# Kernel optimization log

Measured on AMD Instinct MI355X. Metric: run time of the kernel, lower is better.

## Reference

```python
import jax, jax.numpy as jnp
import numpy as np


def setup_inputs() -> dict:
    key = jax.random.key(0)
    k1, k2 = jax.random.split(key)
    x = jax.random.normal(k1, (8, 8192, 512), dtype=jnp.float32)
    codebook = jax.random.normal(k2, (1024, 512), dtype=jnp.float32)
    return {"x": x, "codebook": codebook}


def reference(x, codebook):
    # torch.cdist -> Euclidean distance; argmin is invariant under sqrt, so
    x2 = jnp.sum(x * x, axis=-1, keepdims=True)          # [B, N, 1]
    c2 = jnp.sum(codebook * codebook, axis=-1)           # [K]
    xc = jnp.einsum('bnd,kd->bnk', x, codebook)          # [B, N, K]
    d2 = x2 - 2.0 * xc + c2                              # [B, N, K]
    idx = jnp.argmin(d2, axis=-1)                        # [B, N]
    return codebook[idx]                                 # [B, N, dim]
```

## Files before the change

### kernel.cpp

```cpp
#include <hip/hip_runtime.h>
#include <cstdio>


typedef float f32x4 __attribute__((ext_vector_type(4)));
typedef _Float16 half8 __attribute__((ext_vector_type(8)));

#define KDIM 512
#define NCODES 1024
#define NQ 65536
#define TAU_S 0.05f

#define WS_CBH   0ull
#define WS_C2H   1048576ull
#define WS_C2D   1052672ull
#define WS_CBT   1060864ull
#define WS_IDX   3158016ull
#define WS_LIST  3420160ull
#define WS_CTR   3682304ull
#define WS_NEED  (WS_CTR + 4ull)

__device__ __forceinline__ unsigned short f2h(float f) {
  _Float16 h = (_Float16)f;
  return __builtin_bit_cast(unsigned short, h);
}

__device__ __forceinline__ void async16(const void* g, void* l) {
  __builtin_amdgcn_global_load_lds(
      (const __attribute__((address_space(1))) void*)g,
      (__attribute__((address_space(3))) void*)l, 16, 0, 0);
}

__global__ __launch_bounds__(256) void vq_prep(const float* __restrict__ cb,
                                               unsigned short* __restrict__ cbh,
                                               float* __restrict__ c2h,
                                               double* __restrict__ c2d) {
  int lane = threadIdx.x & 63;
  int row = blockIdx.x * 4 + (threadIdx.x >> 6);
  const float4* src = (const float4*)(cb + (size_t)row * KDIM);
  float4 u = src[lane * 2], v = src[lane * 2 + 1];
  double p = (double)u.x * u.x + (double)u.y * u.y + (double)u.z * u.z + (double)u.w * u.w +
             (double)v.x * v.x + (double)v.y * v.y + (double)v.z * v.z + (double)v.w * v.w;
#pragma unroll
  for (int m = 1; m < 64; m <<= 1) p += __shfl_xor(p, m);
  if (lane == 0) { c2h[row] = (float)(0.5 * p); c2d[row] = 0.5 * p; }
  unsigned r0 = f2h(u.x) | ((unsigned)f2h(u.y) << 16);
  unsigned r1 = f2h(u.z) | ((unsigned)f2h(u.w) << 16);
  unsigned r2 = f2h(v.x) | ((unsigned)f2h(v.y) << 16);
  unsigned r3 = f2h(v.z) | ((unsigned)f2h(v.w) << 16);
  *(int4*)(cbh + (size_t)row * KDIM + lane * 8) = make_int4((int)r0, (int)r1, (int)r2, (int)r3);
}

__global__ __launch_bounds__(512, 2) void vq_main(const float* __restrict__ x,
                                                  const unsigned short* __restrict__ cbh,
                                                  const float* __restrict__ c2h,
                                                  int* __restrict__ idx,
                                                  int* __restrict__ list,
                                                  int* __restrict__ counter) {
  __shared__ __align__(16) char pool[135168];
  float* c2s = (float*)(pool + 131072);

  const int tid = threadIdx.x;
  const int lane = tid & 63, wv = tid >> 6;
  const int c = lane & 15, q = lane >> 4;
  const int qbase = blockIdx.x * 256 + wv * 32;

#define STAGE(cc) do {                                                        \
    const unsigned short* _s = cbh + (size_t)(cc) * 32768 + wv * 4096;        \
    char* _d = pool + (((cc) & 1) * 65536) + wv * 8192 + lane * 16;           \
    _Pragma("unroll")                                                         \
    for (int s = 0; s < 8; ++s)                                               \
      async16(_s + s * 512 + ((lane ^ s) * 8), _d + s * 1024); } while (0)

  if (wv < 4) async16(c2h + (wv * 64 + lane) * 4, pool + 131072 + wv * 1024 + lane * 16);
  STAGE(0);

  half8 a[2][16];
  {
    const float* xr0 = x + (size_t)(qbase + c) * KDIM + q * 8;
    const float* xr1 = xr0 + (size_t)16 * KDIM;
    float4 t0[8], t1[8];
#pragma unroll
    for (int gj = 0; gj < 4; ++gj) {
      const float* p = xr0 + gj * 32;
      t0[gj * 2] = *(const float4*)p;
      t0[gj * 2 + 1] = *(const float4*)(p + 4);
    }
#pragma unroll
    for (int g = 0; g < 8; ++g) {
      if (g + 1 < 8) {
#pragma unroll
        for (int gj = 0; gj < 4; ++gj) {
          const int fi = (g + 1) * 4 + gj;
          const int rf = fi >> 4, kf = fi & 15;
          const float* p = (rf ? xr1 : xr0) + kf * 32;
          if ((g + 1) & 1) {
            t1[gj * 2] = *(const float4*)p; t1[gj * 2 + 1] = *(const float4*)(p + 4);
          } else {
            t0[gj * 2] = *(const float4*)p; t0[gj * 2 + 1] = *(const float4*)(p + 4);
          }
        }
      }
#pragma unroll
      for (int gj = 0; gj < 4; ++gj) {
        const int fi = g * 4 + gj;
        const int rf = fi >> 4, kf = fi & 15;
        float4 lo, hi;
        if (g & 1) { lo = t1[gj * 2]; hi = t1[gj * 2 + 1]; }
        else       { lo = t0[gj * 2]; hi = t0[gj * 2 + 1]; }
        half8 h;
        h[0] = (_Float16)lo.x; h[1] = (_Float16)lo.y;
        h[2] = (_Float16)lo.z; h[3] = (_Float16)lo.w;
        h[4] = (_Float16)hi.x; h[5] = (_Float16)hi.y;
        h[6] = (_Float16)hi.z; h[7] = (_Float16)hi.w;
        a[rf][kf] = h;
      }
      __builtin_amdgcn_sched_barrier(0);
    }
  }

  float m1[2][4], m2[2][4];
  int mcx[2][4];
#pragma unroll
  for (int i = 0; i < 2; ++i)
#pragma unroll
    for (int r = 0; r < 4; ++r) { m1[i][r] = 1e30f; m2[i][r] = 1e30f; mcx[i][r] = 0; }

  const int crow = c * 512;
  const int m3 = c & 7;

#pragma unroll 1
  for (int ch = 0; ch < 16; ++ch) {
    __syncthreads();
    if (ch + 1 < 16) STAGE(ch + 1);

    const unsigned short* B = (const unsigned short*)(pool + ((ch & 1) * 65536));
    f32x4 acc[2][4];
#pragma unroll
    for (int i = 0; i < 2; ++i)
#pragma unroll
      for (int j = 0; j < 4; ++j) acc[i][j] = (f32x4){0.f, 0.f, 0.f, 0.f};

#pragma unroll
    for (int kf = 0; kf < 16; ++kf) {
      half8 b[4];
      const int gg = (kf * 4 + q) ^ m3;
#pragma unroll
      for (int cf = 0; cf < 4; ++cf)
        b[cf] = *(const half8*)&B[cf * 8192 + crow + gg * 8];
#pragma unroll
      for (int i = 0; i < 2; ++i)
#pragma unroll
        for (int cf = 0; cf < 4; ++cf)
          acc[i][cf] = __builtin_amdgcn_mfma_f32_16x16x32_f16(a[i][kf], b[cf], acc[i][cf], 0, 0, 0);
    }
#pragma unroll
    for (int cf = 0; cf < 4; ++cf) {
      const int col = ch * 64 + cf * 16 + c;
      const float c2v = c2s[col];
#pragma unroll
      for (int i = 0; i < 2; ++i)
#pragma unroll
        for (int r = 0; r < 4; ++r) {
          float sv = c2v - acc[i][cf][r];
          float hi = fmaxf(sv, m1[i][r]);
          m2[i][r] = fminf(m2[i][r], hi);
          bool lt = sv < m1[i][r];
          m1[i][r] = lt ? sv : m1[i][r];
          mcx[i][r] = lt ? col : mcx[i][r];
        }
    }
  }
#undef STAGE

#pragma unroll
  for (int m = 1; m < 16; m <<= 1) {
#pragma unroll
    for (int i = 0; i < 2; ++i)
#pragma unroll
      for (int r = 0; r < 4; ++r) {
        float o1 = __shfl_xor(m1[i][r], m);
        float o2 = __shfl_xor(m2[i][r], m);
        int   oc = __shfl_xor(mcx[i][r], m);
        float hi = fmaxf(o1, m1[i][r]);
        m2[i][r] = fminf(fminf(m2[i][r], o2), hi);
        bool lt = o1 < m1[i][r];
        m1[i][r] = lt ? o1 : m1[i][r];
        mcx[i][r] = lt ? oc : mcx[i][r];
      }
  }
  if (c == 0) {
#pragma unroll
    for (int i = 0; i < 2; ++i)
#pragma unroll
      for (int r = 0; r < 4; ++r) {
        int query = qbase + i * 16 + q * 4 + r;
        idx[query] = mcx[i][r];
        if (m2[i][r] - m1[i][r] < TAU_S) { int p = atomicAdd(counter, 1); list[p] = query; }
      }
  }
}

__global__ __launch_bounds__(256) void vq_trans(const float4* __restrict__ cb4,
                                                float4* __restrict__ cbT4) {
  __shared__ float t[64][65];
  const int bc = blockIdx.x >> 3, bk = blockIdx.x & 7;
  const int c0 = bc * 64, k0 = bk * 64;
  const int r = threadIdx.x >> 4, q4 = threadIdx.x & 15;
#pragma unroll
  for (int p = 0; p < 4; ++p) {
    int row = p * 16 + r;
    float4 v = cb4[(size_t)(c0 + row) * 128 + (k0 >> 2) + q4];
    t[row][q4 * 4 + 0] = v.x; t[row][q4 * 4 + 1] = v.y;
    t[row][q4 * 4 + 2] = v.z; t[row][q4 * 4 + 3] = v.w;
  }
  __syncthreads();
#pragma unroll
  for (int p = 0; p < 4; ++p) {
    int kk = p * 16 + r;
    float4 v = make_float4(t[q4 * 4 + 0][kk], t[q4 * 4 + 1][kk],
                           t[q4 * 4 + 2][kk], t[q4 * 4 + 3][kk]);
    cbT4[(size_t)(k0 + kk) * 256 + (c0 >> 2) + q4] = v;
  }
}

__global__ __launch_bounds__(256) void vq_refine(const float* __restrict__ x,
                                                 const float4* __restrict__ cbT4,
                                                 const double* __restrict__ c2d,
                                                 const int* __restrict__ list,
                                                 const int* __restrict__ counter,
                                                 int* __restrict__ idx) {
  __shared__ __align__(16) float xs[8][512];
  __shared__ int qlist[8];
  __shared__ double rv[8][4];
  __shared__ int rc[8][4];
  const int cnt = counter[0];
  const int tid = threadIdx.x, lane = tid & 63, wv = tid >> 6;
  for (int base = blockIdx.x * 8; base < cnt; base += gridDim.x * 8) {
    const int nq = min(8, cnt - base);
    __syncthreads();
    if (tid < 8) qlist[tid] = list[base + ((tid < nq) ? tid : 0)];
    __syncthreads();
#pragma unroll
    for (int k = 0; k < 4; ++k) {
      int e = tid + 256 * k;
      int qi = e >> 7, d4 = e & 127;
      ((float4*)xs)[e] = ((const float4*)(x + (size_t)qlist[qi] * KDIM))[d4];
    }
    __syncthreads();
    double a0[8], a1[8], a2[8], a3[8];
#pragma unroll
    for (int qi = 0; qi < 8; ++qi) { a0[qi] = 0; a1[qi] = 0; a2[qi] = 0; a3[qi] = 0; }
#pragma unroll 2
    for (int k4 = 0; k4 < 128; ++k4) {
      float4 c0 = cbT4[(k4 * 4 + 0) * 256 + tid];
      float4 c1 = cbT4[(k4 * 4 + 1) * 256 + tid];
      float4 c2v = cbT4[(k4 * 4 + 2) * 256 + tid];
      float4 c3 = cbT4[(k4 * 4 + 3) * 256 + tid];
#pragma unroll
      for (int qi = 0; qi < 8; ++qi) {
        float4 xv = *(const float4*)&xs[qi][k4 * 4];
        a0[qi] = fma((double)xv.x, (double)c0.x, a0[qi]);
        a1[qi] = fma((double)xv.x, (double)c0.y, a1[qi]);
        a2[qi] = fma((double)xv.x, (double)c0.z, a2[qi]);
        a3[qi] = fma((double)xv.x, (double)c0.w, a3[qi]);
        a0[qi] = fma((double)xv.y, (double)c1.x, a0[qi]);
        a1[qi] = fma((double)xv.y, (double)c1.y, a1[qi]);
        a2[qi] = fma((double)xv.y, (double)c1.z, a2[qi]);
        a3[qi] = fma((double)xv.y, (double)c1.w, a3[qi]);
        a0[qi] = fma((double)xv.z, (double)c2v.x, a0[qi]);
        a1[qi] = fma((double)xv.z, (double)c2v.y, a1[qi]);
        a2[qi] = fma((double)xv.z, (double)c2v.z, a2[qi]);
        a3[qi] = fma((double)xv.z, (double)c2v.w, a3[qi]);
        a0[qi] = fma((double)xv.w, (double)c3.x, a0[qi]);
        a1[qi] = fma((double)xv.w, (double)c3.y, a1[qi]);
        a2[qi] = fma((double)xv.w, (double)c3.z, a2[qi]);
        a3[qi] = fma((double)xv.w, (double)c3.w, a3[qi]);
      }
    }
    const double c2l0 = c2d[tid * 4], c2l1 = c2d[tid * 4 + 1];
    const double c2l2 = c2d[tid * 4 + 2], c2l3 = c2d[tid * 4 + 3];
#pragma unroll
    for (int qi = 0; qi < 8; ++qi) {
      double best = c2l0 - a0[qi];
      int bc = tid * 4;
      double s1 = c2l1 - a1[qi];
      if (s1 < best) { best = s1; bc = tid * 4 + 1; }
      double s2 = c2l2 - a2[qi];
      if (s2 < best) { best = s2; bc = tid * 4 + 2; }
      double s3 = c2l3 - a3[qi];
      if (s3 < best) { best = s3; bc = tid * 4 + 3; }
#pragma unroll
      for (int m = 1; m < 64; m <<= 1) {
        double o = __shfl_xor(best, m);
        int oc = __shfl_xor(bc, m);
        if (o < best) { best = o; bc = oc; }
      }
      if (lane == 0) { rv[qi][wv] = best; rc[qi][wv] = bc; }
    }
    __syncthreads();
    if (tid < nq) {
      double b = rv[tid][0];
      int bci = rc[tid][0];
#pragma unroll
      for (int w = 1; w < 4; ++w)
        if (rv[tid][w] < b) { b = rv[tid][w]; bci = rc[tid][w]; }
      idx[qlist[tid]] = bci;
    }
  }
}

__global__ __launch_bounds__(256) void vq_gather(const float* __restrict__ cb,
                                                 const int* __restrict__ idx,
                                                 float* __restrict__ out) {
  size_t i = (size_t)blockIdx.x * 256 + threadIdx.x;
  int qg = (int)(i >> 7), d = (int)(i & 127);
  ((float4*)out)[i] = ((const float4*)cb)[(size_t)idx[qg] * 128 + d];
}

extern "C" void kernel_launch(void* const* d_in, const int* in_sizes, int n_in,
                              void* d_out, int out_size, void* d_ws, size_t ws_size,
                              hipStream_t stream) {
  const float* x = (const float*)d_in[0];
  const float* cb = (const float*)d_in[1];
  float* out = (float*)d_out;
  char* ws = (char*)d_ws;
  if (ws_size < WS_NEED) {
    fprintf(stderr, "vq: ws_size %zu too small (need %llu)\n", ws_size,
            (unsigned long long)WS_NEED);
    return;
  }
  unsigned short* cbh = (unsigned short*)(ws + WS_CBH);
  float* c2h = (float*)(ws + WS_C2H);
  double* c2d = (double*)(ws + WS_C2D);
  float* cbT = (float*)(ws + WS_CBT);
  int* idx = (int*)(ws + WS_IDX);
  int* list = (int*)(ws + WS_LIST);
  int* counter = (int*)(ws + WS_CTR);

  hipMemsetAsync(counter, 0, 4, stream);
  vq_prep<<<256, 256, 0, stream>>>(cb, cbh, c2h, c2d);
  vq_trans<<<128, 256, 0, stream>>>((const float4*)cb, (float4*)cbT);
  vq_main<<<256, 512, 0, stream>>>(x, cbh, c2h, idx, list, counter);
  vq_refine<<<2048, 256, 0, stream>>>(x, (const float4*)cbT, c2d, list, counter, idx);
  vq_gather<<<32768, 256, 0, stream>>>(cb, idx, out);
}
```

Before: 418.6 us.

## Give each wave 64 queries in main kernel and simplify refine to one query per block

The main kernel drops to 4 waves per block, and each wave now computes 64 queries instead of 32. This doubles the reuse of every codebook fragment read from LDS but raises register pressure (a[4][16] and acc[4][4]). The x preload loses its software-pipelined double buffering, and staging is rewritten so each wave copies 16 rows. The refine kernel now handles one query per block instead of batching 8, which drops cross-query reuse of the transposed codebook loads.

```diff
diff --git a/kernel.cpp b/kernel.cpp
--- a/kernel.cpp
+++ b/kernel.cpp
@@ -50,7 +50,7 @@
   *(int4*)(cbh + (size_t)row * KDIM + lane * 8) = make_int4((int)r0, (int)r1, (int)r2, (int)r3);
 }
 
-__global__ __launch_bounds__(512, 2) void vq_main(const float* __restrict__ x,
+__global__ __launch_bounds__(256, 1) void vq_main(const float* __restrict__ x,
                                                   const unsigned short* __restrict__ cbh,
                                                   const float* __restrict__ c2h,
                                                   int* __restrict__ idx,
@@ -62,70 +62,51 @@
   const int tid = threadIdx.x;
   const int lane = tid & 63, wv = tid >> 6;
   const int c = lane & 15, q = lane >> 4;
-  const int qbase = blockIdx.x * 256 + wv * 32;
+  const int qbase = blockIdx.x * 256 + wv * 64;
 
 #define STAGE(cc) do {                                                        \
-    const unsigned short* _s = cbh + (size_t)(cc) * 32768 + wv * 4096;        \
-    char* _d = pool + (((cc) & 1) * 65536) + wv * 8192 + lane * 16;           \
+    const unsigned short* _s = cbh + (size_t)(cc) * 32768;                    \
+    char* _d = pool + (((cc) & 1) * 65536);                                   \
     _Pragma("unroll")                                                         \
-    for (int s = 0; s < 8; ++s)                                               \
-      async16(_s + s * 512 + ((lane ^ s) * 8), _d + s * 1024); } while (0)
-
-  if (wv < 4) async16(c2h + (wv * 64 + lane) * 4, pool + 131072 + wv * 1024 + lane * 16);
+    for (int s = 0; s < 16; ++s) {                                            \
+      int r = wv * 16 + s;                                                    \
+      async16(_s + (size_t)r * 512 + ((lane ^ (r & 7)) * 8),                  \
+              _d + r * 1024 + lane * 16);                                     \
+    } } while (0)
+
+  async16(c2h + wv * 256 + lane * 4, pool + 131072 + wv * 1024 + lane * 16);
   STAGE(0);
 
-  half8 a[2][16];
-  {
-    const float* xr0 = x + (size_t)(qbase + c) * KDIM + q * 8;
-    const float* xr1 = xr0 + (size_t)16 * KDIM;
-    float4 t0[8], t1[8];
-#pragma unroll
-    for (int gj = 0; gj < 4; ++gj) {
-      const float* p = xr0 + gj * 32;
-      t0[gj * 2] = *(const float4*)p;
-      t0[gj * 2 + 1] = *(const float4*)(p + 4);
-    }
-#pragma unroll
-    for (int g = 0; g < 8; ++g) {
-      if (g + 1 < 8) {
-#pragma unroll
-        for (int gj = 0; gj < 4; ++gj) {
-          const int fi = (g + 1) * 4 + gj;
-          const int rf = fi >> 4, kf = fi & 15;
-          const float* p = (rf ? xr1 : xr0) + kf * 32;
-          if ((g + 1) & 1) {
-            t1[gj * 2] = *(const float4*)p; t1[gj * 2 + 1] = *(const float4*)(p + 4);
-          } else {
-            t0[gj * 2] = *(const float4*)p; t0[gj * 2 + 1] = *(const float4*)(p + 4);
-          }
-        }
-      }
-#pragma unroll
-      for (int gj = 0; gj < 4; ++gj) {
-        const int fi = g * 4 + gj;
-        const int rf = fi >> 4, kf = fi & 15;
-        float4 lo, hi;
-        if (g & 1) { lo = t1[gj * 2]; hi = t1[gj * 2 + 1]; }
-        else       { lo = t0[gj * 2]; hi = t0[gj * 2 + 1]; }
-        half8 h;
-        h[0] = (_Float16)lo.x; h[1] = (_Float16)lo.y;
-        h[2] = (_Float16)lo.z; h[3] = (_Float16)lo.w;
-        h[4] = (_Float16)hi.x; h[5] = (_Float16)hi.y;
-        h[6] = (_Float16)hi.z; h[7] = (_Float16)hi.w;
-        a[rf][kf] = h;
-      }
-      __builtin_amdgcn_sched_barrier(0);
-    }
-  }
-
-  float m1[2][4], m2[2][4];
-  int mcx[2][4];
-#pragma unroll
-  for (int i = 0; i < 2; ++i)
+  half8 a[4][16];
+#pragma unroll
+  for (int rf = 0; rf < 4; ++rf) {
+    const float* xr = x + (size_t)(qbase + rf * 16 + c) * KDIM + q * 8;
+    float4 t[32];
+#pragma unroll
+    for (int kf = 0; kf < 16; ++kf) {
+      t[kf * 2]     = *(const float4*)(xr + kf * 32);
+      t[kf * 2 + 1] = *(const float4*)(xr + kf * 32 + 4);
+    }
+#pragma unroll
+    for (int kf = 0; kf < 16; ++kf) {
+      float4 lo = t[kf * 2], hi = t[kf * 2 + 1];
+      half8 h;
+      h[0] = (_Float16)lo.x; h[1] = (_Float16)lo.y;
+      h[2] = (_Float16)lo.z; h[3] = (_Float16)lo.w;
+      h[4] = (_Float16)hi.x; h[5] = (_Float16)hi.y;
+      h[6] = (_Float16)hi.z; h[7] = (_Float16)hi.w;
+      a[rf][kf] = h;
+    }
+    __builtin_amdgcn_sched_barrier(0);
+  }
+
+  float m1[4][4], m2[4][4];
+  int mcx[4][4];
+#pragma unroll
+  for (int i = 0; i < 4; ++i)
 #pragma unroll
     for (int r = 0; r < 4; ++r) { m1[i][r] = 1e30f; m2[i][r] = 1e30f; mcx[i][r] = 0; }
 
-  const int crow = c * 512;
   const int m3 = c & 7;
 
 #pragma unroll 1
@@ -134,9 +115,9 @@
     if (ch + 1 < 16) STAGE(ch + 1);
 
     const unsigned short* B = (const unsigned short*)(pool + ((ch & 1) * 65536));
-    f32x4 acc[2][4];
-#pragma unroll
-    for (int i = 0; i < 2; ++i)
+    f32x4 acc[4][4];
+#pragma unroll
+    for (int i = 0; i < 4; ++i)
 #pragma unroll
       for (int j = 0; j < 4; ++j) acc[i][j] = (f32x4){0.f, 0.f, 0.f, 0.f};
 
@@ -146,9 +127,9 @@
       const int gg = (kf * 4 + q) ^ m3;
 #pragma unroll
       for (int cf = 0; cf < 4; ++cf)
-        b[cf] = *(const half8*)&B[cf * 8192 + crow + gg * 8];
-#pragma unroll
-      for (int i = 0; i < 2; ++i)
+        b[cf] = *(const half8*)&B[(cf * 16 + c) * 512 + gg * 8];
+#pragma unroll
+      for (int i = 0; i < 4; ++i)
 #pragma unroll
         for (int cf = 0; cf < 4; ++cf)
           acc[i][cf] = __builtin_amdgcn_mfma_f32_16x16x32_f16(a[i][kf], b[cf], acc[i][cf], 0, 0, 0);
@@ -158,7 +139,7 @@
       const int col = ch * 64 + cf * 16 + c;
       const float c2v = c2s[col];
 #pragma unroll
-      for (int i = 0; i < 2; ++i)
+      for (int i = 0; i < 4; ++i)
 #pragma unroll
         for (int r = 0; r < 4; ++r) {
           float sv = c2v - acc[i][cf][r];
@@ -175,7 +156,7 @@
 #pragma unroll
   for (int m = 1; m < 16; m <<= 1) {
 #pragma unroll
-    for (int i = 0; i < 2; ++i)
+    for (int i = 0; i < 4; ++i)
 #pragma unroll
       for (int r = 0; r < 4; ++r) {
         float o1 = __shfl_xor(m1[i][r], m);
@@ -190,7 +171,7 @@
   }
   if (c == 0) {
 #pragma unroll
-    for (int i = 0; i < 2; ++i)
+    for (int i = 0; i < 4; ++i)
 #pragma unroll
       for (int r = 0; r < 4; ++r) {
         int query = qbase + i * 16 + q * 4 + r;
@@ -229,83 +210,67 @@
                                                  const int* __restrict__ list,
                                                  const int* __restrict__ counter,
                                                  int* __restrict__ idx) {
-  __shared__ __align__(16) float xs[8][512];
-  __shared__ int qlist[8];
-  __shared__ double rv[8][4];
-  __shared__ int rc[8][4];
+  __shared__ float xs[512];
+  __shared__ double rv[4];
+  __shared__ int rc[4];
   const int cnt = counter[0];
   const int tid = threadIdx.x, lane = tid & 63, wv = tid >> 6;
-  for (int base = blockIdx.x * 8; base < cnt; base += gridDim.x * 8) {
-    const int nq = min(8, cnt - base);
-    __syncthreads();
-    if (tid < 8) qlist[tid] = list[base + ((tid < nq) ? tid : 0)];
-    __syncthreads();
-#pragma unroll
-    for (int k = 0; k < 4; ++k) {
-      int e = tid + 256 * k;
-      int qi = e >> 7, d4 = e & 127;
-      ((float4*)xs)[e] = ((const float4*)(x + (size_t)qlist[qi] * KDIM))[d4];
-    }
-    __syncthreads();
-    double a0[8], a1[8], a2[8], a3[8];
-#pragma unroll
-    for (int qi = 0; qi < 8; ++qi) { a0[qi] = 0; a1[qi] = 0; a2[qi] = 0; a3[qi] = 0; }
-#pragma unroll 2
+  for (int qi = blockIdx.x; qi < cnt; qi += gridDim.x) {
+    const int query = list[qi];
+    __syncthreads();
+    xs[tid] = x[(size_t)query * KDIM + tid];
+    xs[tid + 256] = x[(size_t)query * KDIM + tid + 256];
+    __syncthreads();
+    double a0 = 0, a1 = 0, a2 = 0, a3 = 0;
+    const float4* xs4 = (const float4*)xs;
+#pragma unroll 4
     for (int k4 = 0; k4 < 128; ++k4) {
+      float4 xv = xs4[k4];
       float4 c0 = cbT4[(k4 * 4 + 0) * 256 + tid];
       float4 c1 = cbT4[(k4 * 4 + 1) * 256 + tid];
       float4 c2v = cbT4[(k4 * 4 + 2) * 256 + tid];
       float4 c3 = cbT4[(k4 * 4 + 3) * 256 + tid];
-#pragma unroll
-      for (int qi = 0; qi < 8; ++qi) {
-        float4 xv = *(const float4*)&xs[qi][k4 * 4];
-        a0[qi] = fma((double)xv.x, (double)c0.x, a0[qi]);
-        a1[qi] = fma((double)xv.x, (double)c0.y, a1[qi]);
-        a2[qi] = fma((double)xv.x, (double)c0.z, a2[qi]);
-        a3[qi] = fma((double)xv.x, (double)c0.w, a3[qi]);
-        a0[qi] = fma((double)xv.y, (double)c1.x, a0[qi]);
-        a1[qi] = fma((double)xv.y, (double)c1.y, a1[qi]);
-        a2[qi] = fma((double)xv.y, (double)c1.z, a2[qi]);
-        a3[qi] = fma((double)xv.y, (double)c1.w, a3[qi]);
-        a0[qi] = fma((double)xv.z, (double)c2v.x, a0[qi]);
-        a1[qi] = fma((double)xv.z, (double)c2v.y, a1[qi]);
-        a2[qi] = fma((double)xv.z, (double)c2v.z, a2[qi]);
-        a3[qi] = fma((double)xv.z, (double)c2v.w, a3[qi]);
-        a0[qi] = fma((double)xv.w, (double)c3.x, a0[qi]);
-        a1[qi] = fma((double)xv.w, (double)c3.y, a1[qi]);
-        a2[qi] = fma((double)xv.w, (double)c3.z, a2[qi]);
-        a3[qi] = fma((double)xv.w, (double)c3.w, a3[qi]);
-      }
-    }
-    const double c2l0 = c2d[tid * 4], c2l1 = c2d[tid * 4 + 1];
-    const double c2l2 = c2d[tid * 4 + 2], c2l3 = c2d[tid * 4 + 3];
-#pragma unroll
-    for (int qi = 0; qi < 8; ++qi) {
-      double best = c2l0 - a0[qi];
-      int bc = tid * 4;
-      double s1 = c2l1 - a1[qi];
-      if (s1 < best) { best = s1; bc = tid * 4 + 1; }
-      double s2 = c2l2 - a2[qi];
-      if (s2 < best) { best = s2; bc = tid * 4 + 2; }
-      double s3 = c2l3 - a3[qi];
-      if (s3 < best) { best = s3; bc = tid * 4 + 3; }
-#pragma unroll
-      for (int m = 1; m < 64; m <<= 1) {
-        double o = __shfl_xor(best, m);
-        int oc = __shfl_xor(bc, m);
-        if (o < best) { best = o; bc = oc; }
-      }
-      if (lane == 0) { rv[qi][wv] = best; rc[qi][wv] = bc; }
-    }
-    __syncthreads();
-    if (tid < nq) {
-      double b = rv[tid][0];
-      int bci = rc[tid][0];
+      a0 = fma((double)xv.x, (double)c0.x, a0);
+      a1 = fma((double)xv.x, (double)c0.y, a1);
+      a2 = fma((double)xv.x, (double)c0.z, a2);
+      a3 = fma((double)xv.x, (double)c0.w, a3);
+      a0 = fma((double)xv.y, (double)c1.x, a0);
+      a1 = fma((double)xv.y, (double)c1.y, a1);
+      a2 = fma((double)xv.y, (double)c1.z, a2);
+      a3 = fma((double)xv.y, (double)c1.w, a3);
+      a0 = fma((double)xv.z, (double)c2v.x, a0);
+      a1 = fma((double)xv.z, (double)c2v.y, a1);
+      a2 = fma((double)xv.z, (double)c2v.z, a2);
+      a3 = fma((double)xv.z, (double)c2v.w, a3);
+      a0 = fma((double)xv.w, (double)c3.x, a0);
+      a1 = fma((double)xv.w, (double)c3.y, a1);
+      a2 = fma((double)xv.w, (double)c3.z, a2);
+      a3 = fma((double)xv.w, (double)c3.w, a3);
+    }
+    double best = c2d[tid * 4] - a0;
+    int bc = tid * 4;
+    double s1 = c2d[tid * 4 + 1] - a1;
+    if (s1 < best) { best = s1; bc = tid * 4 + 1; }
+    double s2 = c2d[tid * 4 + 2] - a2;
+    if (s2 < best) { best = s2; bc = tid * 4 + 2; }
+    double s3 = c2d[tid * 4 + 3] - a3;
+    if (s3 < best) { best = s3; bc = tid * 4 + 3; }
+#pragma unroll
+    for (int m = 1; m < 64; m <<= 1) {
+      double o = __shfl_xor(best, m);
+      int oc = __shfl_xor(bc, m);
+      if (o < best) { best = o; bc = oc; }
+    }
+    if (lane == 0) { rv[wv] = best; rc[wv] = bc; }
+    __syncthreads();
+    if (tid == 0) {
+      double b = rv[0]; int bci = rc[0];
 #pragma unroll
       for (int w = 1; w < 4; ++w)
-        if (rv[tid][w] < b) { b = rv[tid][w]; bci = rc[tid][w]; }
-      idx[qlist[tid]] = bci;
-    }
+        if (rv[w] < b) { b = rv[w]; bci = rc[w]; }
+      idx[query] = bci;
+    }
+    __syncthreads();
   }
 }
 
@@ -340,7 +305,7 @@
   hipMemsetAsync(counter, 0, 4, stream);
   vq_prep<<<256, 256, 0, stream>>>(cb, cbh, c2h, c2d);
   vq_trans<<<128, 256, 0, stream>>>((const float4*)cb, (float4*)cbT);
-  vq_main<<<256, 512, 0, stream>>>(x, cbh, c2h, idx, list, counter);
+  vq_main<<<256, 256, 0, stream>>>(x, cbh, c2h, idx, list, counter);
   vq_refine<<<2048, 256, 0, stream>>>(x, (const float4*)cbT, c2d, list, counter, idx);
   vq_gather<<<32768, 256, 0, stream>>>(cb, idx, out);
 }
```

Result: faster. 401.6 us (-4.1%).
